# Optimization experiments

Measured on AMD Instinct MI355X. Metric: run time of the kernel, lower is better.

Reference implementation:

```python
import jax, jax.numpy as jnp
import numpy as np
import math

B, C, N, M = 4, 512, 4096, 4096
DA = C // 4
BN_EPS = 1e-5

def setup_inputs() -> dict:
    key = jax.random.key(0)
    ks = jax.random.split(key, 10)
    s = 0.02
    return {
        "x": jax.random.normal(ks[0], (B, C, N), jnp.float32),
        "y": jax.random.normal(ks[1], (B, C, M), jnp.float32),
        # q_conv.weight is tied to k_conv.weight -> single shared [da, C] (no bias)
        "w_qk": jax.random.normal(ks[2], (DA, C), jnp.float32) * s,
        "w_v": jax.random.normal(ks[3], (C, C), jnp.float32) * s,
        "b_v": jax.random.normal(ks[4], (C,), jnp.float32) * s,
        "w_t": jax.random.normal(ks[5], (C, C), jnp.float32) * s,
        "b_t": jax.random.normal(ks[6], (C,), jnp.float32) * s,
        # BatchNorm1d (eval mode: use running stats)
        "gamma": jnp.ones((C,), jnp.float32),
        "beta": jnp.zeros((C,), jnp.float32),
        "run_mean": jax.random.normal(ks[7], (C,), jnp.float32) * 0.1,
        "run_var": jax.random.uniform(ks[8], (C,), jnp.float32, 0.5, 1.5),
    }

def reference(x, y, w_qk, w_v, b_v, w_t, b_t, gamma, beta, run_mean, run_var):
    scale = 1.0 / math.sqrt(DA)
    # 1x1 conv projections (shared q/k weight)
    q = jnp.einsum("dc,bcn->bdn", w_qk, x)                      # [B, da, N]
    k = jnp.einsum("dc,bcm->bdm", w_qk, y)                      # [B, da, M]
    v = jnp.einsum("oc,bcm->bom", w_v, y) + b_v[None, :, None]  # [B, C, M]
    energy = jnp.einsum("bdn,bdm->bnm", q, k) * scale           # [B, N, M]
    attn = jax.nn.softmax(energy, axis=-1)                      # softmax over keys M
    x_s = jnp.einsum("bcm,bnm->bcn", v, attn)                   # [B, C, N]
    x_s = jnp.einsum("oc,bcn->bon", w_t, x_s) + b_t[None, :, None]
    # BatchNorm1d (eval) over channel dim + ReLU
    inv = gamma / jnp.sqrt(run_var + BN_EPS)
    x_s = x_s * inv[None, :, None] + (beta - run_mean * inv)[None, :, None]
    x_s = jax.nn.relu(x_s)
    return jnp.transpose(x_s, (0, 2, 1))                        # [B, N, C]
```

## Files before the change

kernel.cpp:

```cpp
#include <hip/hip_runtime.h>
#include <hip/hip_bf16.h>
#include <stdint.h>

typedef __bf16 bf16;
typedef __bf16 bf16x8 __attribute__((ext_vector_type(8)));
typedef __bf16 bf16x4 __attribute__((ext_vector_type(4)));
typedef float  f32x4  __attribute__((ext_vector_type(4)));

template<typename T> __device__ __forceinline__ bf16x8 load8(const T* p);
template<> __device__ __forceinline__ bf16x8 load8<bf16>(const bf16* p) {
    return *(const bf16x8*)p;
}
template<> __device__ __forceinline__ bf16x8 load8<float>(const float* p) {
    f32x4 a = ((const f32x4*)p)[0];
    f32x4 b = ((const f32x4*)p)[1];
    bf16x8 r;
    #pragma unroll
    for (int m = 0; m < 4; m++) { r[m] = (bf16)a[m]; r[m + 4] = (bf16)b[m]; }
    return r;
}


__device__ __forceinline__ void gld16(bf16* lds, const bf16* g) {
    __builtin_amdgcn_global_load_lds(
        (const __attribute__((address_space(1))) void*)g,
        (__attribute__((address_space(3))) void*)lds, 16, 0, 0);
}

template<int ROWS>
__device__ __forceinline__ void stage(bf16* lds, const bf16* g, int64_t ld, int t) {
    constexpr int NI = ROWS / 32;
    const int w = t >> 6, l = t & 63;
    #pragma unroll
    for (int it = 0; it < NI; it++) {
        const int cb  = (it * 4 + w) * 64;
        const int c   = cb + l;
        const int row = c >> 3, col8 = (c & 7) ^ (row & 7);
        gld16(lds + (int64_t)cb * 8, g + (int64_t)row * ld + col8 * 8);
    }
}

__device__ __forceinline__ bf16x8 frag(const bf16* lds, int row, int g8) {
    return *(const bf16x8*)&lds[(row << 6) + ((g8 ^ (row & 7)) << 3)];
}

template<int BN_>
__device__ __forceinline__ void core_nt(bf16* As, bf16* Bs,
    const bf16* __restrict__ Ab, const bf16* __restrict__ Bb,
    int64_t ldA, int64_t ldB, int kbeg, int kend, f32x4 (*acc)[BN_ / 32])
{
    const int t = threadIdx.x, lane = t & 63, w = t >> 6;
    const int wi = (w >> 1) * 64, wj = (w & 1) * (BN_ / 2);
    const int quad = lane >> 4, l15 = lane & 15;
    for (int k0 = kbeg; k0 < kend; k0 += 64) {
        stage<128>(As, Ab + k0, ldA, t);
        stage<BN_>(Bs, Bb + k0, ldB, t);
        __syncthreads();
        #pragma unroll
        for (int kk = 0; kk < 64; kk += 32) {
            bf16x8 af[4], bfr[BN_ / 32];
            #pragma unroll
            for (int ti = 0; ti < 4; ti++)
                af[ti] = frag(As, wi + ti * 16 + l15, (kk >> 3) + quad);
            #pragma unroll
            for (int tj = 0; tj < BN_ / 32; tj++)
                bfr[tj] = frag(Bs, wj + tj * 16 + l15, (kk >> 3) + quad);
            #pragma unroll
            for (int ti = 0; ti < 4; ti++)
                #pragma unroll
                for (int tj = 0; tj < BN_ / 32; tj++)
                    acc[ti][tj] = __builtin_amdgcn_mfma_f32_16x16x32_bf16(
                        af[ti], bfr[tj], acc[ti][tj], 0, 0, 0);
        }
        __syncthreads();
    }
}

__global__ __launch_bounds__(256) void k_gemm_plain(
    const bf16* __restrict__ A, const bf16* __restrict__ Bm, bf16* __restrict__ Cc,
    int64_t sAz, int64_t sBz, int64_t sCz, int ldA, int ldB, int ldC, int K)
{
    __shared__ bf16 As[128 * 64];
    __shared__ bf16 Bs[128 * 64];
    const int i0 = blockIdx.y * 128, j0 = blockIdx.x * 128;
    const bf16* Ab = A  + blockIdx.z * sAz + (int64_t)i0 * ldA;
    const bf16* Bb = Bm + blockIdx.z * sBz + (int64_t)j0 * ldB;
    f32x4 acc[4][4] = {};
    core_nt<128>(As, Bs, Ab, Bb, ldA, ldB, 0, K, acc);

    bf16* Cb = Cc + blockIdx.z * sCz;
    const int lane = threadIdx.x & 63, w = threadIdx.x >> 6;
    const int wi = (w >> 1) * 64, wj = (w & 1) * 64, quad = lane >> 4, l15 = lane & 15;
    #pragma unroll
    for (int ti = 0; ti < 4; ti++)
        #pragma unroll
        for (int tj = 0; tj < 4; tj++) {
            const int jg = j0 + wj + tj * 16 + l15;
            #pragma unroll
            for (int r = 0; r < 4; r++)
                Cb[(int64_t)(i0 + wi + ti * 16 + quad * 4 + r) * ldC + jg] = (bf16)acc[ti][tj][r];
        }
}

__global__ __launch_bounds__(256) void k_eng(
    const bf16* __restrict__ Q, const bf16* __restrict__ Kt,
    bf16* __restrict__ P, float* __restrict__ L,
    int64_t sQz, int64_t sKz, int64_t sPz, int64_t sLz, int ldQ, int ldK, int ldP, int Kd)
{
    __shared__ bf16 As[128 * 64];
    __shared__ bf16 Bs[128 * 64];
    const int i0 = blockIdx.y * 128, j0 = blockIdx.x * 128;
    const bf16* Ab = Q  + blockIdx.z * sQz + (int64_t)i0 * ldQ;
    const bf16* Bb = Kt + blockIdx.z * sKz + (int64_t)j0 * ldK;
    f32x4 acc[4][4] = {};
    core_nt<128>(As, Bs, Ab, Bb, ldQ, ldK, 0, Kd, acc);

    bf16*  Pb = P + blockIdx.z * sPz;
    float* Lb = L + blockIdx.z * sLz;
    const int lane = threadIdx.x & 63, w = threadIdx.x >> 6;
    const int wi = (w >> 1) * 64, wj = (w & 1) * 64, quad = lane >> 4, l15 = lane & 15;
    #pragma unroll
    for (int ti = 0; ti < 4; ti++) {
        #pragma unroll
        for (int r = 0; r < 4; r++) {
            const int ig = i0 + wi + ti * 16 + quad * 4 + r;
            float s = 0.f;
            #pragma unroll
            for (int tj = 0; tj < 4; tj++) {
                const float e = __expf(acc[ti][tj][r]);
                s += e;
                Pb[(int64_t)ig * ldP + j0 + wj + tj * 16 + l15] = (bf16)e;
            }
            #pragma unroll
            for (int m = 1; m < 16; m <<= 1) s += __shfl_xor(s, m, 64);
            if (l15 == 0) atomicAdd(&Lb[ig], s);
        }
    }
}

__global__ __launch_bounds__(256) void k_recip(float* __restrict__ L, int n) {
    const int i = blockIdx.x * 256 + threadIdx.x;
    if (i < n) L[i] = 1.f / L[i];
}

template<bool PART>
__global__ __launch_bounds__(256) void k_z(
    const bf16* __restrict__ P, const bf16* __restrict__ Y, void* __restrict__ Zout,
    const float* __restrict__ Linv,
    int64_t sPz, int64_t sYz, int64_t sZz, int64_t sLz, int K, int KS)
{
    __shared__ bf16 As[128 * 64];
    __shared__ bf16 Bs[128 * 64];
    const int z = blockIdx.z;
    const int bz = z / KS, ks = z - bz * KS;
    const int i0 = blockIdx.y * 128, j0 = blockIdx.x * 128;
    const bf16* Ab = P + bz * sPz + (int64_t)i0 * K;
    const bf16* Bb = Y + bz * sYz + (int64_t)j0 * K;
    f32x4 acc[4][4] = {};
    const int KR = K / KS;
    core_nt<128>(As, Bs, Ab, Bb, K, K, ks * KR, ks * KR + KR, acc);

    const int lane = threadIdx.x & 63, w = threadIdx.x >> 6;
    const int wi = (w >> 1) * 64, wj = (w & 1) * 64, quad = lane >> 4, l15 = lane & 15;
    #pragma unroll
    for (int ti = 0; ti < 4; ti++)
        #pragma unroll
        for (int tj = 0; tj < 4; tj++) {
            const int jg = j0 + wj + tj * 16 + l15;
            #pragma unroll
            for (int r = 0; r < 4; r++) {
                const int ig = i0 + wi + ti * 16 + quad * 4 + r;
                if constexpr (PART)
                    ((float*)Zout)[(int64_t)ks * sZz + (int64_t)ig * 512 + jg] = acc[ti][tj][r];
                else
                    ((bf16*)Zout)[(int64_t)bz * sZz + (int64_t)ig * 512 + jg] =
                        (bf16)(acc[ti][tj][r] * Linv[bz * sLz + ig]);
            }
        }
}

__global__ __launch_bounds__(256) void k_zred(const float* __restrict__ Zp,
    bf16* __restrict__ Z, const float* __restrict__ Linv, int64_t n, int64_t slice, int KS)
{
    const int64_t idx = ((int64_t)blockIdx.x * 256 + threadIdx.x) * 8;
    if (idx >= n) return;
    f32x4 a0 = {}, a1 = {};
    for (int s = 0; s < KS; s++) {
        const float* p = Zp + (int64_t)s * slice + idx;
        a0 += *(const f32x4*)p;
        a1 += *(const f32x4*)(p + 4);
    }
    const float sc = Linv[idx >> 9];
    bf16x8 o;
    #pragma unroll
    for (int m = 0; m < 4; m++) { o[m] = (bf16)(a0[m] * sc); o[m + 4] = (bf16)(a1[m] * sc); }
    *(bf16x8*)&Z[idx] = o;
}

__global__ __launch_bounds__(256) void k_out(const int* __restrict__ flag,
    const bf16* __restrict__ Z, const bf16* __restrict__ W, void* __restrict__ outB,
    int64_t sZz, int64_t row0, int64_t rowz,
    const float* __restrict__ bias2,
    const void* gma, const void* bta, const void* mean, const void* var)
{
    __shared__ bf16 As[128 * 64];
    __shared__ bf16 Bs[128 * 64];
    const int i0 = blockIdx.y * 128, j0 = blockIdx.x * 128;
    const bf16* Ab = Z + blockIdx.z * sZz + (int64_t)i0 * 512;
    const bf16* Bb = W + (int64_t)j0 * 512;
    f32x4 acc[4][4] = {};
    core_nt<128>(As, Bs, Ab, Bb, 512, 512, 0, 512, acc);

    const int f = *flag;
    const int lane = threadIdx.x & 63, w = threadIdx.x >> 6;
    const int wi = (w >> 1) * 64, wj = (w & 1) * 64, quad = lane >> 4, l15 = lane & 15;
    const int64_t rbase = row0 + (int64_t)blockIdx.z * rowz;
    #pragma unroll
    for (int ti = 0; ti < 4; ti++)
        #pragma unroll
        for (int tj = 0; tj < 4; tj++) {
            const int jg = j0 + wj + tj * 16 + l15;
            float g, be, mn, vr;
            if (f) {
                g  = ((const float*)gma)[jg];  be = ((const float*)bta)[jg];
                mn = ((const float*)mean)[jg]; vr = ((const float*)var)[jg];
            } else {
                g  = (float)((const bf16*)gma)[jg];  be = (float)((const bf16*)bta)[jg];
                mn = (float)((const bf16*)mean)[jg]; vr = (float)((const bf16*)var)[jg];
            }
            const float inv = g * rsqrtf(vr + 1e-5f);
            const float add = be - mn * inv;
            const float bj  = bias2[jg];
            #pragma unroll
            for (int r = 0; r < 4; r++) {
                const int ig = i0 + wi + ti * 16 + quad * 4 + r;
                float val = (acc[ti][tj][r] + bj) * inv + add;
                val = fmaxf(val, 0.f);
                if (f) ((float*)outB)[(rbase + ig) * 512 + jg] = val;
                else   ((bf16*)outB)[(rbase + ig) * 512 + jg] = (bf16)val;
            }
        }
}

template<typename TA>
__device__ __forceinline__ void proj_core(bf16 (*As)[72], bf16 (*Bs)[72],
    const TA* __restrict__ Ag, const bf16* __restrict__ Bg, int64_t ldA, f32x4 (*acc)[4])
{
    const int t = threadIdx.x, lane = t & 63, w = t >> 6;
    const int wi = (w >> 1) * 64, wj = (w & 1) * 64;
    const int quad = lane >> 4, l15 = lane & 15;
    for (int k0 = 0; k0 < 512; k0 += 64) {
        #pragma unroll
        for (int gi = 0; gi < 4; gi++) {
            const int c = t * 4 + gi, k = c >> 4, i8 = c & 15;
            bf16x8 v = load8<TA>(Ag + (int64_t)(k0 + k) * ldA + i8 * 8);
            #pragma unroll
            for (int m = 0; m < 8; m++) As[i8 * 8 + m][k] = v[m];
        }
        #pragma unroll
        for (int gi = 0; gi < 4; gi++) {
            const int c = t * 4 + gi, r = c >> 3, kg = c & 7;
            *(bf16x8*)&Bs[r][kg * 8] = *(const bf16x8*)(Bg + r * 512 + k0 + kg * 8);
        }
        __syncthreads();
        #pragma unroll
        for (int kk = 0; kk < 64; kk += 32) {
            bf16x8 af[4], bfr[4];
            #pragma unroll
            for (int ti = 0; ti < 4; ti++)
                af[ti] = *(const bf16x8*)&As[wi + ti * 16 + l15][kk + quad * 8];
            #pragma unroll
            for (int tj = 0; tj < 4; tj++)
                bfr[tj] = *(const bf16x8*)&Bs[wj + tj * 16 + l15][kk + quad * 8];
            #pragma unroll
            for (int ti = 0; ti < 4; ti++)
                #pragma unroll
                for (int tj = 0; tj < 4; tj++)
                    acc[ti][tj] = __builtin_amdgcn_mfma_f32_16x16x32_bf16(
                        af[ti], bfr[tj], acc[ti][tj], 0, 0, 0);
        }
        __syncthreads();
    }
}

__global__ __launch_bounds__(256) void k_proj(const int* __restrict__ flag,
    const void* __restrict__ X, int64_t sX, const bf16* __restrict__ wqk,
    bf16* __restrict__ Q, int64_t sQ, int ldX, float scale)
{
    __shared__ bf16 As[128][72];
    __shared__ bf16 Bs[128][72];
    const int i0 = blockIdx.y * 128;
    f32x4 acc[4][4] = {};
    if (*flag)
        proj_core<float>(As, Bs, (const float*)X + blockIdx.z * sX + i0, wqk, ldX, acc);
    else
        proj_core<bf16>(As, Bs, (const bf16*)X + blockIdx.z * sX + i0, wqk, ldX, acc);

    bf16* C = Q + blockIdx.z * sQ;
    const int lane = threadIdx.x & 63, w = threadIdx.x >> 6;
    const int wi = (w >> 1) * 64, wj = (w & 1) * 64, quad = lane >> 4, l15 = lane & 15;
    #pragma unroll
    for (int ti = 0; ti < 4; ti++)
        #pragma unroll
        for (int tj = 0; tj < 4; tj++) {
            const int jg = wj + tj * 16 + l15;
            #pragma unroll
            for (int r = 0; r < 4; r++) {
                const int ig = i0 + wi + ti * 16 + quad * 4 + r;
                C[(int64_t)ig * 128 + jg] = (bf16)(acc[ti][tj][r] * scale);
            }
        }
}

__global__ void k_detect(const void* gma, int* flag) {
    if (threadIdx.x == 0 && blockIdx.x == 0) {
        uint16_t h = ((const uint16_t*)gma)[0];
        *flag = (h == 0x3F80u) ? 0 : 1;
    }
}

__global__ __launch_bounds__(256) void k_cvt(const int* __restrict__ flag,
    const void* __restrict__ in, bf16* __restrict__ outp, int64_t n)
{
    const int64_t idx = ((int64_t)blockIdx.x * 256 + threadIdx.x) * 8;
    if (idx >= n) return;
    bf16x8 v = (*flag) ? load8<float>((const float*)in + idx)
                       : load8<bf16>((const bf16*)in + idx);
    *(bf16x8*)&outp[idx] = v;
}

__global__ __launch_bounds__(256) void k_tr(const int* __restrict__ flag,
    const void* __restrict__ in, bf16* __restrict__ outp, int R, int Cc)
{
    __shared__ float tile[64][65];
    const int r0 = blockIdx.y * 64, c0 = blockIdx.x * 64;
    const int t = threadIdx.x;
    const int rl = t >> 4, cl = (t & 15) * 4;
    const int f = *flag;
    #pragma unroll
    for (int p = 0; p < 4; p++) {
        const int r = rl + p * 16;
        if (f) {
            f32x4 v = *(const f32x4*)((const float*)in + (int64_t)(r0 + r) * Cc + c0 + cl);
            #pragma unroll
            for (int m = 0; m < 4; m++) tile[r][cl + m] = v[m];
        } else {
            const bf16* q = (const bf16*)in + (int64_t)(r0 + r) * Cc + c0 + cl;
            #pragma unroll
            for (int m = 0; m < 4; m++) tile[r][cl + m] = (float)q[m];
        }
    }
    __syncthreads();
    #pragma unroll
    for (int p = 0; p < 4; p++) {
        const int crow = rl + p * 16;
        bf16x4 o;
        #pragma unroll
        for (int m = 0; m < 4; m++) o[m] = (bf16)tile[cl + m][crow];
        *(bf16x4*)(outp + (int64_t)(c0 + crow) * R + r0 + cl) = o;
    }
}

__global__ __launch_bounds__(256) void k_bias2(const int* __restrict__ flag,
    const void* bv, const void* wt, const void* bt, float* __restrict__ bias2)
{
    const int o = blockIdx.x, t = threadIdx.x;
    const int f = *flag;
    float s = 0.f;
    for (int c = t; c < 512; c += 256) {
        float b, wv;
        if (f) { b = ((const float*)bv)[c]; wv = ((const float*)wt)[(int64_t)o * 512 + c]; }
        else   { b = (float)((const bf16*)bv)[c]; wv = (float)((const bf16*)wt)[(int64_t)o * 512 + c]; }
        s += b * wv;
    }
    #pragma unroll
    for (int off = 1; off < 64; off <<= 1) s += __shfl_xor(s, off, 64);
    __shared__ float red[4];
    if ((t & 63) == 0) red[t >> 6] = s;
    __syncthreads();
    if (t == 0) {
        float tot = red[0] + red[1] + red[2] + red[3];
        float btv = f ? ((const float*)bt)[o] : (float)((const bf16*)bt)[o];
        bias2[o] = tot + btv;
    }
}

extern "C" void kernel_launch(void* const* d_in, const int* in_sizes, int n_in,
                              void* d_out, int out_size, void* d_ws, size_t ws_size,
                              hipStream_t stream)
{
    constexpr int B = 4, C = 512, N = 4096, M = 4096, DA = 128;
    const float scale = 0.08838834764831845f;

    const void* x    = d_in[0];
    const void* y    = d_in[1];
    const void* w_qk = d_in[2];
    const void* w_v  = d_in[3];
    const void* b_v  = d_in[4];
    const void* w_t  = d_in[5];
    const void* b_t  = d_in[6];
    const void* gma  = d_in[7];
    const void* bta  = d_in[8];
    const void* rmean= d_in[9];
    const void* rvar = d_in[10];

    char* ws = (char*)d_ws;
    size_t off = 0;
    auto take = [&](size_t nbytes) { size_t p = off; off = (off + nbytes + 255) & ~(size_t)255; return p; };
    int*   flag  = (int*)  (ws + take(4));
    float* bias2 = (float*)(ws + take(512 * 4));
    bf16*  wqkb  = (bf16*) (ws + take((size_t)DA * C * 2));
    bf16*  wtb   = (bf16*) (ws + take((size_t)C * C * 2));
    bf16*  wvT   = (bf16*) (ws + take((size_t)C * C * 2));
    bf16*  W     = (bf16*) (ws + take((size_t)C * C * 2));
    bf16*  qT    = (bf16*) (ws + take((size_t)B * N * DA * 2));
    bf16*  kT    = (bf16*) (ws + take((size_t)B * M * DA * 2));
    bf16*  yb    = (bf16*) (ws + take((size_t)B * C * M * 2));
    if (off > ws_size) return;
    const size_t rem = ws_size - off;

    int bsz = 1, chunk = 0, KS = 1;
    if      (rem >= (size_t)4 * N * ((M + C) * 2 + 4)) { bsz = 4; chunk = N; }
    else if (rem >= (size_t)2 * N * ((M + C) * 2 + 4)) { bsz = 2; chunk = N; }
    else {
        const int candC[] = {4096, 2048, 4096, 1024, 2048, 512, 1024, 256, 512, 128, 256, 128};
        const int candK[] = {4,    4,    1,    4,    1,    4,   1,    4,   1,   4,   1,   1};
        for (int i = 0; i < 12; i++) {
            size_t need = (size_t)candC[i] * ((M + C) * 2 + 4)
                        + (candK[i] > 1 ? (size_t)candK[i] * candC[i] * C * 4 : 0);
            if (need <= rem) { chunk = candC[i]; KS = candK[i]; break; }
        }
        if (!chunk) return;
    }

    bf16*  P  = (bf16*) (ws + take((size_t)bsz * chunk * M * 2));
    bf16*  Z  = (bf16*) (ws + take((size_t)bsz * chunk * C * 2));
    float* L  = (float*)(ws + take((size_t)bsz * chunk * 4));
    float* Zp = nullptr;
    if (KS > 1) Zp = (float*)(ws + take((size_t)KS * chunk * C * 4));
    if (off > ws_size) return;

    dim3 blk(256);

    k_detect<<<1, 64, 0, stream>>>(gma, flag);
    k_cvt<<<dim3((DA * C) / 2048), blk, 0, stream>>>(flag, w_qk, wqkb, (int64_t)DA * C);
    k_cvt<<<dim3((C * C) / 2048), blk, 0, stream>>>(flag, w_t, wtb, (int64_t)C * C);
    k_cvt<<<dim3((unsigned)(((size_t)B * C * M) / 2048)), blk, 0, stream>>>(
        flag, y, yb, (int64_t)B * C * M);
    k_tr<<<dim3(C / 64, C / 64), blk, 0, stream>>>(flag, w_v, wvT, C, C);
    k_gemm_plain<<<dim3(C / 128, C / 128, 1), blk, 0, stream>>>(
        wtb, wvT, W, 0, 0, 0, C, C, C, C);
    k_bias2<<<C, blk, 0, stream>>>(flag, b_v, w_t, b_t, bias2);

    k_proj<<<dim3(1, N / 128, B), blk, 0, stream>>>(
        flag, x, (int64_t)C * N, wqkb, qT, (int64_t)N * DA, N, scale);
    k_proj<<<dim3(1, M / 128, B), blk, 0, stream>>>(
        flag, y, (int64_t)C * M, wqkb, kT, (int64_t)M * DA, M, 1.f);

    for (int b0 = 0; b0 < B; b0 += bsz) {
        for (int n0 = 0; n0 < N; n0 += chunk) {
            const int nrows = bsz * chunk;
            hipMemsetAsync(L, 0, (size_t)nrows * 4, stream);

            k_eng<<<dim3(M / 128, chunk / 128, bsz), blk, 0, stream>>>(
                qT + ((size_t)b0 * N + n0) * DA, kT + (size_t)b0 * M * DA, P, L,
                (int64_t)N * DA, (int64_t)M * DA, (int64_t)chunk * M, (int64_t)chunk,
                DA, DA, M, DA);

            k_recip<<<(nrows + 255) / 256, blk, 0, stream>>>(L, nrows);

            if (KS > 1) {
                k_z<true><<<dim3(C / 128, chunk / 128, bsz * KS), blk, 0, stream>>>(
                    P, yb + (size_t)b0 * C * M, Zp, L,
                    (int64_t)chunk * M, (int64_t)C * M, (int64_t)chunk * C, (int64_t)chunk,
                    M, KS);
                k_zred<<<dim3((unsigned)(((size_t)chunk * C) / 2048)), blk, 0, stream>>>(
                    Zp, Z, L, (int64_t)chunk * C, (int64_t)chunk * C, KS);
            } else {
                k_z<false><<<dim3(C / 128, chunk / 128, bsz), blk, 0, stream>>>(
                    P, yb + (size_t)b0 * C * M, Z, L,
                    (int64_t)chunk * M, (int64_t)C * M, (int64_t)chunk * C, (int64_t)chunk,
                    M, 1);
            }

            k_out<<<dim3(C / 128, chunk / 128, bsz), blk, 0, stream>>>(
                flag, Z, W, d_out, (int64_t)chunk * C, (int64_t)b0 * N + n0, (int64_t)N,
                bias2, gma, bta, rmean, rvar);
        }
    }

    (void)in_sizes; (void)n_in; (void)out_size;
}
```

Measured before the change: 360.4 us.

## Fuse attention into flash-style kernel with pre-folded value-output projection

Replaces the materialized energy/P matrix pipeline (k_eng, k_recip, k_z, k_out) with one fused kernel that computes exp scores per key tile, keeps P in LDS, and multiplies directly by a precomputed V' = (W_t·W_v)·y. The folded projection is applied to y up front (k_vw), so the per-query output GEMM and the large P/Z intermediates in global memory go away. No running max is subtracted in the softmax, as before. V fragments are read straight from global memory inside the loop, and the kernel relies on 512-thread blocks with two blocks per CU.

```diff
diff --git a/kernel.cpp b/kernel.cpp
--- a/kernel.cpp
+++ b/kernel.cpp
@@ -5,6 +5,7 @@
 typedef __bf16 bf16;
 typedef __bf16 bf16x8 __attribute__((ext_vector_type(8)));
 typedef __bf16 bf16x4 __attribute__((ext_vector_type(4)));
+typedef __bf16 bf16x2 __attribute__((ext_vector_type(2)));
 typedef float  f32x4  __attribute__((ext_vector_type(4)));
 
 template<typename T> __device__ __forceinline__ bf16x8 load8(const T* p);
@@ -34,6 +35,19 @@
     #pragma unroll
     for (int it = 0; it < NI; it++) {
         const int cb  = (it * 4 + w) * 64;
+        const int c   = cb + l;
+        const int row = c >> 3, col8 = (c & 7) ^ (row & 7);
+        gld16(lds + (int64_t)cb * 8, g + (int64_t)row * ld + col8 * 8);
+    }
+}
+
+template<int ROWS>
+__device__ __forceinline__ void stage512(bf16* lds, const bf16* g, int64_t ld, int t) {
+    constexpr int NI = ROWS / 64;
+    const int w = t >> 6, l = t & 63;
+    #pragma unroll
+    for (int it = 0; it < NI; it++) {
+        const int cb  = (it * 8 + w) * 64;
         const int c   = cb + l;
         const int row = c >> 3, col8 = (c & 7) ^ (row & 7);
         gld16(lds + (int64_t)cb * 8, g + (int64_t)row * ld + col8 * 8);
@@ -99,146 +113,6 @@
             #pragma unroll
             for (int r = 0; r < 4; r++)
                 Cb[(int64_t)(i0 + wi + ti * 16 + quad * 4 + r) * ldC + jg] = (bf16)acc[ti][tj][r];
-        }
-}
-
-__global__ __launch_bounds__(256) void k_eng(
-    const bf16* __restrict__ Q, const bf16* __restrict__ Kt,
-    bf16* __restrict__ P, float* __restrict__ L,
-    int64_t sQz, int64_t sKz, int64_t sPz, int64_t sLz, int ldQ, int ldK, int ldP, int Kd)
-{
-    __shared__ bf16 As[128 * 64];
-    __shared__ bf16 Bs[128 * 64];
-    const int i0 = blockIdx.y * 128, j0 = blockIdx.x * 128;
-    const bf16* Ab = Q  + blockIdx.z * sQz + (int64_t)i0 * ldQ;
-    const bf16* Bb = Kt + blockIdx.z * sKz + (int64_t)j0 * ldK;
-    f32x4 acc[4][4] = {};
-    core_nt<128>(As, Bs, Ab, Bb, ldQ, ldK, 0, Kd, acc);
-
-    bf16*  Pb = P + blockIdx.z * sPz;
-    float* Lb = L + blockIdx.z * sLz;
-    const int lane = threadIdx.x & 63, w = threadIdx.x >> 6;
-    const int wi = (w >> 1) * 64, wj = (w & 1) * 64, quad = lane >> 4, l15 = lane & 15;
-    #pragma unroll
-    for (int ti = 0; ti < 4; ti++) {
-        #pragma unroll
-        for (int r = 0; r < 4; r++) {
-            const int ig = i0 + wi + ti * 16 + quad * 4 + r;
-            float s = 0.f;
-            #pragma unroll
-            for (int tj = 0; tj < 4; tj++) {
-                const float e = __expf(acc[ti][tj][r]);
-                s += e;
-                Pb[(int64_t)ig * ldP + j0 + wj + tj * 16 + l15] = (bf16)e;
-            }
-            #pragma unroll
-            for (int m = 1; m < 16; m <<= 1) s += __shfl_xor(s, m, 64);
-            if (l15 == 0) atomicAdd(&Lb[ig], s);
-        }
-    }
-}
-
-__global__ __launch_bounds__(256) void k_recip(float* __restrict__ L, int n) {
-    const int i = blockIdx.x * 256 + threadIdx.x;
-    if (i < n) L[i] = 1.f / L[i];
-}
-
-template<bool PART>
-__global__ __launch_bounds__(256) void k_z(
-    const bf16* __restrict__ P, const bf16* __restrict__ Y, void* __restrict__ Zout,
-    const float* __restrict__ Linv,
-    int64_t sPz, int64_t sYz, int64_t sZz, int64_t sLz, int K, int KS)
-{
-    __shared__ bf16 As[128 * 64];
-    __shared__ bf16 Bs[128 * 64];
-    const int z = blockIdx.z;
-    const int bz = z / KS, ks = z - bz * KS;
-    const int i0 = blockIdx.y * 128, j0 = blockIdx.x * 128;
-    const bf16* Ab = P + bz * sPz + (int64_t)i0 * K;
-    const bf16* Bb = Y + bz * sYz + (int64_t)j0 * K;
-    f32x4 acc[4][4] = {};
-    const int KR = K / KS;
-    core_nt<128>(As, Bs, Ab, Bb, K, K, ks * KR, ks * KR + KR, acc);
-
-    const int lane = threadIdx.x & 63, w = threadIdx.x >> 6;
-    const int wi = (w >> 1) * 64, wj = (w & 1) * 64, quad = lane >> 4, l15 = lane & 15;
-    #pragma unroll
-    for (int ti = 0; ti < 4; ti++)
-        #pragma unroll
-        for (int tj = 0; tj < 4; tj++) {
-            const int jg = j0 + wj + tj * 16 + l15;
-            #pragma unroll
-            for (int r = 0; r < 4; r++) {
-                const int ig = i0 + wi + ti * 16 + quad * 4 + r;
-                if constexpr (PART)
-                    ((float*)Zout)[(int64_t)ks * sZz + (int64_t)ig * 512 + jg] = acc[ti][tj][r];
-                else
-                    ((bf16*)Zout)[(int64_t)bz * sZz + (int64_t)ig * 512 + jg] =
-                        (bf16)(acc[ti][tj][r] * Linv[bz * sLz + ig]);
-            }
-        }
-}
-
-__global__ __launch_bounds__(256) void k_zred(const float* __restrict__ Zp,
-    bf16* __restrict__ Z, const float* __restrict__ Linv, int64_t n, int64_t slice, int KS)
-{
-    const int64_t idx = ((int64_t)blockIdx.x * 256 + threadIdx.x) * 8;
-    if (idx >= n) return;
-    f32x4 a0 = {}, a1 = {};
-    for (int s = 0; s < KS; s++) {
-        const float* p = Zp + (int64_t)s * slice + idx;
-        a0 += *(const f32x4*)p;
-        a1 += *(const f32x4*)(p + 4);
-    }
-    const float sc = Linv[idx >> 9];
-    bf16x8 o;
-    #pragma unroll
-    for (int m = 0; m < 4; m++) { o[m] = (bf16)(a0[m] * sc); o[m + 4] = (bf16)(a1[m] * sc); }
-    *(bf16x8*)&Z[idx] = o;
-}
-
-__global__ __launch_bounds__(256) void k_out(const int* __restrict__ flag,
-    const bf16* __restrict__ Z, const bf16* __restrict__ W, void* __restrict__ outB,
-    int64_t sZz, int64_t row0, int64_t rowz,
-    const float* __restrict__ bias2,
-    const void* gma, const void* bta, const void* mean, const void* var)
-{
-    __shared__ bf16 As[128 * 64];
-    __shared__ bf16 Bs[128 * 64];
-    const int i0 = blockIdx.y * 128, j0 = blockIdx.x * 128;
-    const bf16* Ab = Z + blockIdx.z * sZz + (int64_t)i0 * 512;
-    const bf16* Bb = W + (int64_t)j0 * 512;
-    f32x4 acc[4][4] = {};
-    core_nt<128>(As, Bs, Ab, Bb, 512, 512, 0, 512, acc);
-
-    const int f = *flag;
-    const int lane = threadIdx.x & 63, w = threadIdx.x >> 6;
-    const int wi = (w >> 1) * 64, wj = (w & 1) * 64, quad = lane >> 4, l15 = lane & 15;
-    const int64_t rbase = row0 + (int64_t)blockIdx.z * rowz;
-    #pragma unroll
-    for (int ti = 0; ti < 4; ti++)
-        #pragma unroll
-        for (int tj = 0; tj < 4; tj++) {
-            const int jg = j0 + wj + tj * 16 + l15;
-            float g, be, mn, vr;
-            if (f) {
-                g  = ((const float*)gma)[jg];  be = ((const float*)bta)[jg];
-                mn = ((const float*)mean)[jg]; vr = ((const float*)var)[jg];
-            } else {
-                g  = (float)((const bf16*)gma)[jg];  be = (float)((const bf16*)bta)[jg];
-                mn = (float)((const bf16*)mean)[jg]; vr = (float)((const bf16*)var)[jg];
-            }
-            const float inv = g * rsqrtf(vr + 1e-5f);
-            const float add = be - mn * inv;
-            const float bj  = bias2[jg];
-            #pragma unroll
-            for (int r = 0; r < 4; r++) {
-                const int ig = i0 + wi + ti * 16 + quad * 4 + r;
-                float val = (acc[ti][tj][r] + bj) * inv + add;
-                val = fmaxf(val, 0.f);
-                if (f) ((float*)outB)[(rbase + ig) * 512 + jg] = val;
-                else   ((bf16*)outB)[(rbase + ig) * 512 + jg] = (bf16)val;
-            }
         }
 }
 
@@ -308,6 +182,175 @@
             for (int r = 0; r < 4; r++) {
                 const int ig = i0 + wi + ti * 16 + quad * 4 + r;
                 C[(int64_t)ig * 128 + jg] = (bf16)(acc[ti][tj][r] * scale);
+            }
+        }
+}
+
+__global__ __launch_bounds__(256) void k_vw(const int* __restrict__ flag,
+    const void* __restrict__ Y, int64_t sY, const bf16* __restrict__ Wm,
+    bf16* __restrict__ Vout, int64_t sV, int ldY)
+{
+    __shared__ bf16 As[128][72];
+    __shared__ bf16 Bs[128][72];
+    const int i0 = blockIdx.y * 128;
+    const int o0 = blockIdx.x * 128;
+    f32x4 acc[4][4] = {};
+    if (*flag)
+        proj_core<float>(As, Bs, (const float*)Y + blockIdx.z * sY + i0, Wm + (int64_t)o0 * 512, ldY, acc);
+    else
+        proj_core<bf16>(As, Bs, (const bf16*)Y + blockIdx.z * sY + i0, Wm + (int64_t)o0 * 512, ldY, acc);
+
+    bf16* Cb = Vout + blockIdx.z * sV;
+    const int lane = threadIdx.x & 63, w = threadIdx.x >> 6;
+    const int wi = (w >> 1) * 64, wj = (w & 1) * 64, quad = lane >> 4, l15 = lane & 15;
+    #pragma unroll
+    for (int ti = 0; ti < 4; ti++)
+        #pragma unroll
+        for (int tj = 0; tj < 4; tj++) {
+            const int o = o0 + wj + tj * 16 + l15;
+            const int m = i0 + wi + ti * 16 + quad * 4;
+            bf16x4 ov;
+            #pragma unroll
+            for (int r = 0; r < 4; r++) ov[r] = (bf16)acc[ti][tj][r];
+            *(bf16x4*)(Cb + (int64_t)o * ldY + m) = ov;
+        }
+}
+
+__global__ __launch_bounds__(512, 2) void k_fa(const int* __restrict__ flag,
+    const bf16* __restrict__ Qg,
+    const bf16* __restrict__ Kg,
+    const bf16* __restrict__ Vg,
+    void* __restrict__ outB,
+    const float* __restrict__ bias2,
+    const void* gma, const void* bta, const void* mean, const void* var)
+{
+    constexpr int DA = 128, M = 4096, N = 4096, MT = 128, NT = M / MT;
+    __shared__ bf16 Ks[2][2][128 * 64];
+    __shared__ bf16 Ps[64][136];
+    __shared__ float Lsh[64];
+
+    const int t = threadIdx.x, lane = t & 63, w = t >> 6;
+    const int quad = lane >> 4, l15 = lane & 15;
+    const int b = blockIdx.y, n0 = blockIdx.x * 64;
+    const int wm = w & 3, wn = w >> 2;
+
+    const bf16* Qb = Qg + ((int64_t)b * N + n0) * DA;
+    const bf16* Kb = Kg + (int64_t)b * M * DA;
+    const bf16* Vb = Vg + (int64_t)b * 512 * M;
+
+    bf16x8 qf[2][4];
+    #pragma unroll
+    for (int tj = 0; tj < 2; tj++)
+        #pragma unroll
+        for (int kk = 0; kk < 4; kk++)
+            qf[tj][kk] = *(const bf16x8*)(Qb + (int64_t)(wn * 32 + tj * 16 + l15) * DA
+                                          + kk * 32 + quad * 8);
+
+    if (t < 64) Lsh[t] = 0.f;
+
+    f32x4 acc[4][4] = {};
+
+    stage512<128>(&Ks[0][0][0], Kb, DA, t);
+    stage512<128>(&Ks[0][1][0], Kb + 64, DA, t);
+    __syncthreads();
+
+    for (int mt = 0; mt < NT; mt++) {
+        const int cur = mt & 1;
+        if (mt + 1 < NT) {
+            const bf16* g = Kb + (int64_t)(mt + 1) * MT * DA;
+            stage512<128>(&Ks[cur ^ 1][0][0], g, DA, t);
+            stage512<128>(&Ks[cur ^ 1][1][0], g + 64, DA, t);
+        }
+        f32x4 sacc[2][2] = {};
+        #pragma unroll
+        for (int kk = 0; kk < 4; kk++) {
+            bf16x8 kf[2];
+            #pragma unroll
+            for (int ti = 0; ti < 2; ti++)
+                kf[ti] = frag(&Ks[cur][kk >> 1][0], wm * 32 + ti * 16 + l15, (kk & 1) * 4 + quad);
+            #pragma unroll
+            for (int ti = 0; ti < 2; ti++)
+                #pragma unroll
+                for (int tj = 0; tj < 2; tj++)
+                    sacc[ti][tj] = __builtin_amdgcn_mfma_f32_16x16x32_bf16(
+                        kf[ti], qf[tj][kk], sacc[ti][tj], 0, 0, 0);
+        }
+        float rsum[2] = {0.f, 0.f};
+        #pragma unroll
+        for (int ti = 0; ti < 2; ti++)
+            #pragma unroll
+            for (int tj = 0; tj < 2; tj++) {
+                const float e0 = __expf(sacc[ti][tj][0]);
+                const float e1 = __expf(sacc[ti][tj][1]);
+                const float e2 = __expf(sacc[ti][tj][2]);
+                const float e3 = __expf(sacc[ti][tj][3]);
+                rsum[tj] += (e0 + e1) + (e2 + e3);
+                const int n  = wn * 32 + tj * 16 + l15;
+                const int mb = wm * 32 + ti * 16 + quad * 4;
+                bf16x2 p01, p23;
+                p01[0] = (bf16)e0; p01[1] = (bf16)e1;
+                p23[0] = (bf16)e2; p23[1] = (bf16)e3;
+                *(bf16x2*)&Ps[n][mb]     = p01;
+                *(bf16x2*)&Ps[n][mb + 2] = p23;
+            }
+        #pragma unroll
+        for (int tj = 0; tj < 2; tj++) {
+            float s = rsum[tj];
+            s += __shfl_xor(s, 16, 64);
+            s += __shfl_xor(s, 32, 64);
+            if (quad == 0) atomicAdd(&Lsh[wn * 32 + tj * 16 + l15], s);
+        }
+        __syncthreads();
+        const int64_t vbase = (int64_t)(w * 64) * M + (int64_t)mt * MT;
+        #pragma unroll
+        for (int ks = 0; ks < 4; ks++) {
+            bf16x8 pf[4], vf[4];
+            #pragma unroll
+            for (int tj = 0; tj < 4; tj++)
+                vf[tj] = *(const bf16x8*)(Vb + vbase + (int64_t)(tj * 16 + l15) * M
+                                          + ks * 32 + quad * 8);
+            #pragma unroll
+            for (int ti = 0; ti < 4; ti++)
+                pf[ti] = *(const bf16x8*)&Ps[ti * 16 + l15][ks * 32 + quad * 8];
+            #pragma unroll
+            for (int ti = 0; ti < 4; ti++)
+                #pragma unroll
+                for (int tj = 0; tj < 4; tj++)
+                    acc[ti][tj] = __builtin_amdgcn_mfma_f32_16x16x32_bf16(
+                        pf[ti], vf[tj], acc[ti][tj], 0, 0, 0);
+        }
+        __syncthreads();
+    }
+
+    const int f = *flag;
+    const int64_t rbase = (int64_t)b * N + n0;
+    float inv4[4], add4[4], bj4[4];
+    int og[4];
+    #pragma unroll
+    for (int tj = 0; tj < 4; tj++) {
+        const int o = w * 64 + tj * 16 + l15;
+        og[tj] = o;
+        float g, be, mn, vr;
+        if (f) { g  = ((const float*)gma)[o];  be = ((const float*)bta)[o];
+                 mn = ((const float*)mean)[o]; vr = ((const float*)var)[o]; }
+        else   { g  = (float)((const bf16*)gma)[o];  be = (float)((const bf16*)bta)[o];
+                 mn = (float)((const bf16*)mean)[o]; vr = (float)((const bf16*)var)[o]; }
+        inv4[tj] = g * rsqrtf(vr + 1e-5f);
+        add4[tj] = be - mn * inv4[tj];
+        bj4[tj]  = bias2[o];
+    }
+    #pragma unroll
+    for (int ti = 0; ti < 4; ti++)
+        #pragma unroll
+        for (int r = 0; r < 4; r++) {
+            const int nl = ti * 16 + quad * 4 + r;
+            const float linv = 1.f / Lsh[nl];
+            #pragma unroll
+            for (int tj = 0; tj < 4; tj++) {
+                float val = (acc[ti][tj][r] * linv + bj4[tj]) * inv4[tj] + add4[tj];
+                val = fmaxf(val, 0.f);
+                if (f) ((float*)outB)[(rbase + nl) * 512 + og[tj]] = val;
+                else   ((bf16*)outB)[(rbase + nl) * 512 + og[tj]] = (bf16)val;
             }
         }
 }
@@ -415,29 +458,7 @@
     bf16*  W     = (bf16*) (ws + take((size_t)C * C * 2));
     bf16*  qT    = (bf16*) (ws + take((size_t)B * N * DA * 2));
     bf16*  kT    = (bf16*) (ws + take((size_t)B * M * DA * 2));
-    bf16*  yb    = (bf16*) (ws + take((size_t)B * C * M * 2));
-    if (off > ws_size) return;
-    const size_t rem = ws_size - off;
-
-    int bsz = 1, chunk = 0, KS = 1;
-    if      (rem >= (size_t)4 * N * ((M + C) * 2 + 4)) { bsz = 4; chunk = N; }
-    else if (rem >= (size_t)2 * N * ((M + C) * 2 + 4)) { bsz = 2; chunk = N; }
-    else {
-        const int candC[] = {4096, 2048, 4096, 1024, 2048, 512, 1024, 256, 512, 128, 256, 128};
-        const int candK[] = {4,    4,    1,    4,    1,    4,   1,    4,   1,   4,   1,   1};
-        for (int i = 0; i < 12; i++) {
-            size_t need = (size_t)candC[i] * ((M + C) * 2 + 4)
-                        + (candK[i] > 1 ? (size_t)candK[i] * candC[i] * C * 4 : 0);
-            if (need <= rem) { chunk = candC[i]; KS = candK[i]; break; }
-        }
-        if (!chunk) return;
-    }
-
-    bf16*  P  = (bf16*) (ws + take((size_t)bsz * chunk * M * 2));
-    bf16*  Z  = (bf16*) (ws + take((size_t)bsz * chunk * C * 2));
-    float* L  = (float*)(ws + take((size_t)bsz * chunk * 4));
-    float* Zp = nullptr;
-    if (KS > 1) Zp = (float*)(ws + take((size_t)KS * chunk * C * 4));
+    bf16*  vW    = (bf16*) (ws + take((size_t)B * C * M * 2));
     if (off > ws_size) return;
 
     dim3 blk(256);
@@ -445,8 +466,6 @@
     k_detect<<<1, 64, 0, stream>>>(gma, flag);
     k_cvt<<<dim3((DA * C) / 2048), blk, 0, stream>>>(flag, w_qk, wqkb, (int64_t)DA * C);
     k_cvt<<<dim3((C * C) / 2048), blk, 0, stream>>>(flag, w_t, wtb, (int64_t)C * C);
-    k_cvt<<<dim3((unsigned)(((size_t)B * C * M) / 2048)), blk, 0, stream>>>(
-        flag, y, yb, (int64_t)B * C * M);
     k_tr<<<dim3(C / 64, C / 64), blk, 0, stream>>>(flag, w_v, wvT, C, C);
     k_gemm_plain<<<dim3(C / 128, C / 128, 1), blk, 0, stream>>>(
         wtb, wvT, W, 0, 0, 0, C, C, C, C);
@@ -457,37 +476,11 @@
     k_proj<<<dim3(1, M / 128, B), blk, 0, stream>>>(
         flag, y, (int64_t)C * M, wqkb, kT, (int64_t)M * DA, M, 1.f);
 
-    for (int b0 = 0; b0 < B; b0 += bsz) {
-        for (int n0 = 0; n0 < N; n0 += chunk) {
-            const int nrows = bsz * chunk;
-            hipMemsetAsync(L, 0, (size_t)nrows * 4, stream);
-
-            k_eng<<<dim3(M / 128, chunk / 128, bsz), blk, 0, stream>>>(
-                qT + ((size_t)b0 * N + n0) * DA, kT + (size_t)b0 * M * DA, P, L,
-                (int64_t)N * DA, (int64_t)M * DA, (int64_t)chunk * M, (int64_t)chunk,
-                DA, DA, M, DA);
-
-            k_recip<<<(nrows + 255) / 256, blk, 0, stream>>>(L, nrows);
-
-            if (KS > 1) {
-                k_z<true><<<dim3(C / 128, chunk / 128, bsz * KS), blk, 0, stream>>>(
-                    P, yb + (size_t)b0 * C * M, Zp, L,
-                    (int64_t)chunk * M, (int64_t)C * M, (int64_t)chunk * C, (int64_t)chunk,
-                    M, KS);
-                k_zred<<<dim3((unsigned)(((size_t)chunk * C) / 2048)), blk, 0, stream>>>(
-                    Zp, Z, L, (int64_t)chunk * C, (int64_t)chunk * C, KS);
-            } else {
-                k_z<false><<<dim3(C / 128, chunk / 128, bsz), blk, 0, stream>>>(
-                    P, yb + (size_t)b0 * C * M, Z, L,
-                    (int64_t)chunk * M, (int64_t)C * M, (int64_t)chunk * C, (int64_t)chunk,
-                    M, 1);
-            }
-
-            k_out<<<dim3(C / 128, chunk / 128, bsz), blk, 0, stream>>>(
-                flag, Z, W, d_out, (int64_t)chunk * C, (int64_t)b0 * N + n0, (int64_t)N,
-                bias2, gma, bta, rmean, rvar);
-        }
-    }
+    k_vw<<<dim3(C / 128, M / 128, B), blk, 0, stream>>>(
+        flag, y, (int64_t)C * M, W, vW, (int64_t)C * M, M);
+
+    k_fa<<<dim3(N / 64, B), dim3(512), 0, stream>>>(
+        flag, qT, kT, vW, d_out, bias2, gma, bta, rmean, rvar);
 
     (void)in_sizes; (void)n_in; (void)out_size;
 }
```

Result: slower. 382.6 us (+6.2%).
